# Optimization experiments

Hardware: AMD Instinct MI355X
Metric: run time of the kernel (lower is better)

The kernel has to match this reference:

```python
import jax, jax.numpy as jnp
import numpy as np

N_POINTS = 50000
IN_DIM = 16
HID = 64
HEADS = 4
SCALE = 1
NEG_SLOPE = 0.2  # PyG GATConv default
DELTAS = [1, 3, 5, 7, 9, 11]


def _make_graphs(n, scale):
    # edge_index_1: edges (i-d, i); edge_index_2: edges (i+d, i); edge_index_3: both
    e1 = np.concatenate([np.stack([np.arange(d * scale, n) - d * scale,
                                   np.arange(d * scale, n)]) for d in DELTAS], axis=1)
    e2 = np.concatenate([np.stack([np.arange(n - d * scale) + d * scale,
                                   np.arange(n - d * scale)]) for d in DELTAS], axis=1)
    e3 = np.concatenate([e1, e2], axis=1)
    return (jnp.asarray(e1, dtype=jnp.int64), jnp.asarray(e2, dtype=jnp.int64),
            jnp.asarray(e3, dtype=jnp.int64))


def setup_inputs() -> dict:
    key = jax.random.key(0)
    ks = jax.random.split(key, 16)
    e1, e2, e3 = _make_graphs(N_POINTS, SCALE)
    HC = HEADS * HID

    def g(k, shape, fan_in):
        return jax.random.normal(k, shape, dtype=jnp.float32) * (1.0 / np.sqrt(fan_in))

    return {
        "x": jax.random.normal(ks[0], (N_POINTS, IN_DIM), dtype=jnp.float32),
        "edge_index_1": e1,
        "edge_index_2": e2,
        "edge_index_3": e3,
        # stacked params for the 3 branches (leading dim 3)
        "W1": g(ks[1], (3, IN_DIM, HC), IN_DIM),
        "a1_src": g(ks[2], (3, HEADS, HID), HID),
        "a1_dst": g(ks[3], (3, HEADS, HID), HID),
        "b1": jnp.zeros((3, HC), dtype=jnp.float32),
        "W2": g(ks[4], (3, HC, HC), HC),
        "a2_src": g(ks[5], (3, HEADS, HID), HID),
        "a2_dst": g(ks[6], (3, HEADS, HID), HID),
        "b2": jnp.zeros((3, HID), dtype=jnp.float32),
        "W_fc": g(ks[7], (3, HID, 1), HID),
        "b_fc": jnp.zeros((3, 1), dtype=jnp.float32),
    }


def _gat(x, src, dst, W, a_src, a_dst, b, concat):
    """PyG GATConv: linear -> edge attention -> scatter-softmax -> scatter-add."""
    N = x.shape[0]
    H, C = a_src.shape
    h = (x @ W).reshape(N, H, C)                      # [N,H,C]
    # add self loops (PyG default add_self_loops=True; input graphs have none)
    loop = jnp.arange(N, dtype=src.dtype)
    src = jnp.concatenate([src, loop])
    dst = jnp.concatenate([dst, loop])
    alpha_s = (h * a_src).sum(-1)                     # [N,H]
    alpha_d = (h * a_dst).sum(-1)                     # [N,H]
    e = jax.nn.leaky_relu(alpha_s[src] + alpha_d[dst], NEG_SLOPE)  # [E,H]
    m = jax.ops.segment_max(e, dst, num_segments=N)   # per-dst max (stable softmax)
    ex = jnp.exp(e - m[dst])
    den = jax.ops.segment_sum(ex, dst, num_segments=N)
    alpha = ex / den[dst]                             # [E,H]
    out = jax.ops.segment_sum(alpha[:, :, None] * h[src], dst, num_segments=N)  # [N,H,C]
    out = out.reshape(N, H * C) if concat else out.mean(axis=1)
    return out + b


def reference(x, edge_index_1, edge_index_2, edge_index_3,
              W1, a1_src, a1_dst, b1, W2, a2_src, a2_dst, b2, W_fc, b_fc):
    eis = [edge_index_1, edge_index_2, edge_index_3]
    outs = []
    for k in range(3):
        src, dst = eis[k][0], eis[k][1]
        h = _gat(x, src, dst, W1[k], a1_src[k], a1_dst[k], b1[k], concat=True)
        h = _gat(h, src, dst, W2[k], a2_src[k], a2_dst[k], b2[k], concat=False)
        outs.append(h @ W_fc[k] + b_fc[k])            # [N,1]
    return tuple(outs)  # training-mode output (x1, x2, x3)
```

## Files before the change

kernel.cpp:

```cpp
#include <hip/hip_runtime.h>

#define NPTS 50000
#define NEG 0.2f
#define PSTRIDE 960
#define OUT_N 64
#define SPAN 86
#define SP 87
#define LOG2E 1.44269504088896340736f

typedef unsigned short u16;
typedef unsigned int   u32;

__device__ __forceinline__ float bf2f(u16 u){ return __uint_as_float(((u32)u) << 16); }
__device__ __forceinline__ u16 f2bf(float f){
  u32 w = __float_as_uint(f);
  return (u16)((w + 0x7fffu + ((w >> 16) & 1u)) >> 16);
}
__device__ __forceinline__ u32 pk2(float a, float b){
  return (u32)f2bf(a) | ((u32)f2bf(b) << 16);
}
__device__ __forceinline__ float ldraw(const void* p, long i, int isf32){
  return isf32 ? ((const float*)p)[i] : bf2f(((const u16*)p)[i]);
}
__device__ __forceinline__ float wred(float v){
  #pragma unroll
  for (int m = 32; m > 0; m >>= 1) v += __shfl_xor(v, m, 64);
  return v;
}

__device__ int detect_isf32(const void* x){
  int lane = threadIdx.x & 63;
  const u16* p = (const u16*)x;
  int ze = 0, sane = 0;
  #pragma unroll
  for (int r = 0; r < 8; r++){
    int idx = lane * 8 + r;
    u16 u = p[idx];
    if ((idx & 1) == 0 && u == 0) ze++;
    float a = fabsf(bf2f(u));
    if (u == 0 || (a > 0.015625f && a < 64.f)) sane++;
  }
  #pragma unroll
  for (int m = 32; m > 0; m >>= 1){ ze += __shfl_xor(ze, m, 64); sane += __shfl_xor(sane, m, 64); }
  return (ze > 200) ? 1 : (sane > 460 ? 0 : 1);
}

template<int B> __device__ __forceinline__ int nbr_off(int t){
  if (B == 0){ constexpr int O[7]  = {0,-1,-3,-5,-7,-9,-11}; return O[t]; }
  else if (B == 1){ constexpr int O[7]  = {0,1,3,5,7,9,11}; return O[t]; }
  else { constexpr int O[13] = {0,-1,1,-3,3,-5,5,-7,7,-9,9,-11,11}; return O[t]; }
}

__global__ __launch_bounds__(256) void k_fold1(const void* x, const void* W2, const void* a2s,
                                               const void* a2d, const void* wfc, float* sAg,
                                               int* flag){
  __shared__ int s_flag;
  if (threadIdx.x < 64){ int f = detect_isf32(x); if (threadIdx.x == 0) s_flag = f; }
  __syncthreads();
  int isf32 = s_flag;
  if (blockIdx.x == 0 && blockIdx.y == 0 && threadIdx.x == 0) *flag = isf32;
  int kb = blockIdx.y, m = blockIdx.x;
  int hp = threadIdx.x >> 6, ch = threadIdx.x & 63;
  int c = hp * 64 + ch;
  float w = ldraw(W2, (long)kb * 65536 + (long)m * 256 + c, isf32);
  float s = wred(w * ldraw(a2s, kb * 256 + c, isf32));
  float d = wred(w * ldraw(a2d, kb * 256 + c, isf32));
  float f = wred(w * ldraw(wfc, kb * 64 + ch, isf32) * 0.25f);
  if (ch == 0){
    float* sA = sAg + (long)kb * 3072;
    sA[(0 * 4 + hp) * 256 + m] = s;
    sA[(1 * 4 + hp) * 256 + m] = d;
    sA[(2 * 4 + hp) * 256 + m] = f;
  }
}

__global__ __launch_bounds__(256) void k_fold2(const void* x, const void* W1, const void* a1s,
                                               const void* a1d, const void* b1, const void* b2,
                                               const void* wfc, const void* bfc,
                                               const float* sAg, float* P){
  __shared__ int s_flag;
  if (threadIdx.x < 64){ int f = detect_isf32(x); if (threadIdx.x == 0) s_flag = f; }
  __syncthreads();
  int isf32 = s_flag;
  int kb = blockIdx.y;
  int wid = blockIdx.x * 4 + (threadIdx.x >> 6);
  int ch = threadIdx.x & 63;
  float* Pp = P + kb * PSTRIDE;
  const float* sA = sAg + (long)kb * 3072;

  if (wid < 256){
    int hp = wid & 3, h = (wid >> 2) & 3, k = wid >> 4;
    int m = h * 64 + ch;
    float w = ldraw(W1, (long)kb * 4096 + k * 256 + m, isf32);
    float s = wred(w * sA[(0 * 4 + hp) * 256 + m]);
    float d = wred(w * sA[(1 * 4 + hp) * 256 + m]);
    float f = wred(w * sA[(2 * 4 + hp) * 256 + m]);
    if (ch == 0){ Pp[128 + wid] = s; Pp[384 + wid] = d; Pp[640 + wid] = f; }
  } else if (wid < 320){
    int j = wid - 256; int h = j & 3, k = j >> 2;
    int c = h * 64 + ch;
    float w = ldraw(W1, (long)kb * 4096 + k * 256 + c, isf32);
    float s = wred(w * ldraw(a1s, kb * 256 + c, isf32));
    float d = wred(w * ldraw(a1d, kb * 256 + c, isf32));
    if (ch == 0){ Pp[j] = s; Pp[64 + j] = d; }
  } else if (wid < 324){
    int hp = wid - 320;
    float a0 = 0.f, a1v = 0.f, a2v = 0.f;
    for (int it = 0; it < 4; it++){
      int m = it * 64 + ch;
      float bv = ldraw(b1, kb * 256 + m, isf32);
      a0  += bv * sA[(0 * 4 + hp) * 256 + m];
      a1v += bv * sA[(1 * 4 + hp) * 256 + m];
      a2v += bv * sA[(2 * 4 + hp) * 256 + m];
    }
    a0 = wred(a0); a1v = wred(a1v); a2v = wred(a2v);
    if (ch == 0){ Pp[896 + hp] = a0; Pp[900 + hp] = a1v; Pp[904 + hp] = a2v; }
  } else if (wid == 324){
    float a = wred(ldraw(b2, kb * 64 + ch, isf32) * ldraw(wfc, kb * 64 + ch, isf32));
    if (ch == 0) Pp[908] = a + ldraw(bfc, kb, isf32);
  }
}

template<int BRANCH>
__device__ __forceinline__ void run_ab(const void* x, const float* Pp, int isf32, int base,
                                       float (&fe8)[8][SP], u32 (&feG)[4][SP * 7], float* o2b){
  constexpr int CNT = (BRANCH == 2) ? 13 : 7;
  int tid = threadIdx.x;

  if (tid < SPAN){
    int g = base - 11 + tid;
    bool vA = (unsigned)g < NPTS;
    float xv[16];
    if (vA){
      if (isf32){
        const float4* xp = (const float4*)x + (long)g * 4;
        #pragma unroll
        for (int q = 0; q < 4; q++){
          float4 v = xp[q];
          xv[q*4] = v.x; xv[q*4+1] = v.y; xv[q*4+2] = v.z; xv[q*4+3] = v.w;
        }
      } else {
        const uint4* xp = (const uint4*)x + (long)g * 2;
        #pragma unroll
        for (int q = 0; q < 2; q++){
          uint4 v = xp[q];
          u32 wsv[4] = {v.x, v.y, v.z, v.w};
          #pragma unroll
          for (int r = 0; r < 4; r++){
            xv[q*8 + r*2]     = bf2f((u16)(wsv[r] & 0xffffu));
            xv[q*8 + r*2 + 1] = bf2f((u16)(wsv[r] >> 16));
          }
        }
      }
    } else {
      #pragma unroll
      for (int k = 0; k < 16; k++) xv[k] = 0.f;
    }
    float s1[4] = {0,0,0,0}, d1[4] = {0,0,0,0};
    float s2[16], d2[16], f2[16];
    #pragma unroll
    for (int t = 0; t < 16; t++){ s2[t] = 0.f; d2[t] = 0.f; f2[t] = 0.f; }
    #pragma unroll
    for (int k = 0; k < 16; k++){
      float xk = xv[k];
      #pragma unroll
      for (int h = 0; h < 4; h++){
        s1[h] += xk * Pp[     k*4 + h];
        d1[h] += xk * Pp[64 + k*4 + h];
      }
      #pragma unroll
      for (int t = 0; t < 16; t++){
        s2[t] += xk * Pp[128 + k*16 + t];
        d2[t] += xk * Pp[384 + k*16 + t];
        f2[t] += xk * Pp[640 + k*16 + t];
      }
    }
    #pragma unroll
    for (int h = 0; h < 4; h++){
      fe8[h][tid]     = s1[h] * LOG2E;
      fe8[4 + h][tid] = d1[h] * LOG2E;
      u32* gp = &feG[h][tid * 7];
      gp[0] = pk2(s2[h*4+0], s2[h*4+1]);
      gp[1] = pk2(s2[h*4+2], s2[h*4+3]);
      gp[2] = pk2(d2[h*4+0], d2[h*4+1]);
      gp[3] = pk2(d2[h*4+2], d2[h*4+3]);
      gp[4] = pk2(f2[h*4+0], f2[h*4+1]);
      gp[5] = pk2(f2[h*4+2], f2[h*4+3]);
    }
  }
  __syncthreads();

  #pragma unroll
  for (int pass = 0; pass < 2; pass++){
    int task = pass * 128 + tid;
    int noff = task >> 2, h = task & 3;
    int i = base + noff;
    bool vB = i < NPTS;
    float ts[4] = {0,0,0,0}, td[4] = {0,0,0,0}, tf[4] = {0,0,0,0};
    if (vB){
      int sAs = noff + 11;
      float adv = fe8[4 + h][sAs];
      float e[CNT]; int sa[CNT];
      float mx = -3e38f;
      #pragma unroll
      for (int tt = 0; tt < CNT; tt++){
        int off = nbr_off<BRANCH>(tt);
        int j = i + off;
        sa[tt] = sAs + off;
        float v = fe8[h][sa[tt]] + adv;
        v = v > 0.f ? v : NEG * v;
        e[tt] = ((unsigned)j < NPTS) ? v : -3e38f;
        mx = fmaxf(mx, e[tt]);
      }
      float den = 0.f;
      #pragma unroll
      for (int tt = 0; tt < CNT; tt++){
        float ex = exp2f(e[tt] - mx);
        den += ex;
        const u32* gp = &feG[h][sa[tt] * 7];
        u32 g0 = gp[0], g1 = gp[1], g2 = gp[2], g3 = gp[3], g4 = gp[4], g5 = gp[5];
        ts[0] += ex * bf2f((u16)(g0 & 0xffffu)); ts[1] += ex * bf2f((u16)(g0 >> 16));
        ts[2] += ex * bf2f((u16)(g1 & 0xffffu)); ts[3] += ex * bf2f((u16)(g1 >> 16));
        td[0] += ex * bf2f((u16)(g2 & 0xffffu)); td[1] += ex * bf2f((u16)(g2 >> 16));
        td[2] += ex * bf2f((u16)(g3 & 0xffffu)); td[3] += ex * bf2f((u16)(g3 >> 16));
        tf[0] += ex * bf2f((u16)(g4 & 0xffffu)); tf[1] += ex * bf2f((u16)(g4 >> 16));
        tf[2] += ex * bf2f((u16)(g5 & 0xffffu)); tf[3] += ex * bf2f((u16)(g5 >> 16));
      }
      float inv = 1.f / den;
      #pragma unroll
      for (int hp = 0; hp < 4; hp++){ ts[hp] *= inv; td[hp] *= inv; tf[hp] *= inv; }
    }
    #pragma unroll
    for (int hp = 0; hp < 4; hp++){
      ts[hp] += __shfl_xor(ts[hp], 1, 64); ts[hp] += __shfl_xor(ts[hp], 2, 64);
      td[hp] += __shfl_xor(td[hp], 1, 64); td[hp] += __shfl_xor(td[hp], 2, 64);
      tf[hp] += __shfl_xor(tf[hp], 1, 64); tf[hp] += __shfl_xor(tf[hp], 2, 64);
    }
    if (h == 0 && vB){
      float* ob = o2b + (long)i * 12;
      *(float4*)(ob + 0) = make_float4((ts[0] + Pp[896]) * LOG2E, (ts[1] + Pp[897]) * LOG2E,
                                       (ts[2] + Pp[898]) * LOG2E, (ts[3] + Pp[899]) * LOG2E);
      *(float4*)(ob + 4) = make_float4((td[0] + Pp[900]) * LOG2E, (td[1] + Pp[901]) * LOG2E,
                                       (td[2] + Pp[902]) * LOG2E, (td[3] + Pp[903]) * LOG2E);
      *(float4*)(ob + 8) = make_float4(tf[0] + Pp[904], tf[1] + Pp[905],
                                       tf[2] + Pp[906], tf[3] + Pp[907]);
    }
  }
}

__global__ __launch_bounds__(128) void k_AB(const void* x, const float* P, const int* flag,
                                            float* o2g){
  __shared__ float fe8[8][SP];
  __shared__ u32 feG[4][SP * 7];
  int br = blockIdx.y;
  int isf32 = *flag;
  const float* Pp = P + br * PSTRIDE;
  float* o2b = o2g + (long)br * NPTS * 12;
  int base = blockIdx.x * OUT_N;
  if (br == 0)      run_ab<0>(x, Pp, isf32, base, fe8, feG, o2b);
  else if (br == 1) run_ab<1>(x, Pp, isf32, base, fe8, feG, o2b);
  else              run_ab<2>(x, Pp, isf32, base, fe8, feG, o2b);
}

template<int BRANCH>
__device__ __forceinline__ void run_c(const float* ob, const float* Pp, int isf32, long t,
                                      void* out){
  constexpr int CNT = (BRANCH == 2) ? 13 : 7;
  int node = (int)(t >> 2), hp = (int)(t & 3);
  if (node >= NPTS) return;
  float adv = ob[(long)node * 12 + 4 + hp];
  float e[CNT]; int jc[CNT];
  float mx = -3e38f;
  #pragma unroll
  for (int tt = 0; tt < CNT; tt++){
    int off = nbr_off<BRANCH>(tt);
    int j = node + off;
    int jj = j < 0 ? 0 : (j >= NPTS ? NPTS - 1 : j);
    jc[tt] = jj;
    float v = ob[(long)jj * 12 + hp] + adv;
    v = v > 0.f ? v : NEG * v;
    e[tt] = ((unsigned)j < NPTS) ? v : -3e38f;
    mx = fmaxf(mx, e[tt]);
  }
  float den = 0.f, sm = 0.f;
  #pragma unroll
  for (int tt = 0; tt < CNT; tt++){
    float ex = exp2f(e[tt] - mx);
    den += ex;
    sm += ex * ob[(long)jc[tt] * 12 + 8 + hp];
  }
  float r = sm / den;
  r += __shfl_xor(r, 1, 64);
  r += __shfl_xor(r, 2, 64);
  if (hp == 0){
    float o = r + Pp[908];
    long oi = (long)BRANCH * NPTS + node;
    if (isf32) ((float*)out)[oi] = o;
    else       ((u16*)out)[oi]  = f2bf(o);
  }
}

__global__ __launch_bounds__(256) void k_C(const float* o2g, const float* P, const int* flag,
                                           void* out){
  long t = (long)blockIdx.x * 256 + threadIdx.x;
  int br = blockIdx.y;
  int isf32 = *flag;
  const float* ob = o2g + (long)br * NPTS * 12;
  const float* Pp = P + br * PSTRIDE;
  if (br == 0)      run_c<0>(ob, Pp, isf32, t, out);
  else if (br == 1) run_c<1>(ob, Pp, isf32, t, out);
  else              run_c<2>(ob, Pp, isf32, t, out);
}

extern "C" void kernel_launch(void* const* d_in, const int* in_sizes, int n_in,
                              void* d_out, int out_size, void* d_ws, size_t ws_size,
                              hipStream_t stream){
  char* ws = (char*)d_ws;
  size_t off = 0;
  auto take = [&](size_t b) -> size_t { size_t r = off; off += (b + 255) & ~(size_t)255; return r; };

  float* sAg  = (float*)(ws + take((size_t)3 * 3072 * 4));
  float* P    = (float*)(ws + take((size_t)3 * PSTRIDE * 4));
  int*   flag = (int*)(ws + take(4));
  float* o2g  = (float*)(ws + take((size_t)3 * NPTS * 12 * 4));

  const void* x   = d_in[0];
  const void* W1  = d_in[4];
  const void* a1s = d_in[5];
  const void* a1d = d_in[6];
  const void* b1  = d_in[7];
  const void* W2  = d_in[8];
  const void* a2s = d_in[9];
  const void* a2d = d_in[10];
  const void* b2  = d_in[11];
  const void* wfc = d_in[12];
  const void* bfc = d_in[13];

  k_fold1<<<dim3(256, 3), 256, 0, stream>>>(x, W2, a2s, a2d, wfc, sAg, flag);
  k_fold2<<<dim3(82, 3), 256, 0, stream>>>(x, W1, a1s, a1d, b1, b2, wfc, bfc, sAg, P);
  k_AB<<<dim3((NPTS + OUT_N - 1) / OUT_N, 3), 128, 0, stream>>>(x, P, flag, o2g);
  k_C<<<dim3((NPTS * 4 + 255) / 256, 3), 256, 0, stream>>>(o2g, P, flag, d_out);
}
```

Before: 58.94 us.

## Split fused halo-tile AB kernel into per-node feature kernel and gather kernel

Replaces the shared-memory tiled k_AB kernel, which recomputed node features over an 86-node halo for every 64 outputs and used only 128 threads, with two kernels. k_feat computes each node's projected features once and writes them to a global workspace as fp32 attention logits plus packed bf16 values. k_B then gathers neighbor features from global memory, one thread per node-head. The aim is to remove the halo recomputation and raise occupancy, at the cost of an extra launch and a global round trip of about 19 MB. The bf16 packing and unpacking also switch to hardware intrinsics and mask-based shifts.

New measurement: 56.62 us. 1.04x faster.

```diff
diff --git a/kernel.cpp b/kernel.cpp
--- a/kernel.cpp
+++ b/kernel.cpp
@@ -1,11 +1,9 @@
 #include <hip/hip_runtime.h>
+#include <hip/hip_bf16.h>
 
 #define NPTS 50000
 #define NEG 0.2f
 #define PSTRIDE 960
-#define OUT_N 64
-#define SPAN 86
-#define SP 87
 #define LOG2E 1.44269504088896340736f
 
 typedef unsigned short u16;
@@ -17,8 +15,12 @@
   return (u16)((w + 0x7fffu + ((w >> 16) & 1u)) >> 16);
 }
 __device__ __forceinline__ u32 pk2(float a, float b){
-  return (u32)f2bf(a) | ((u32)f2bf(b) << 16);
-}
+  __hip_bfloat162 h2 = __float22bfloat162_rn(float2{a, b});
+  union { __hip_bfloat162 h; u32 u; } cv; cv.h = h2;
+  return cv.u;
+}
+__device__ __forceinline__ float ulo(u32 g){ return __uint_as_float(g << 16); }
+__device__ __forceinline__ float uhi(u32 g){ return __uint_as_float(g & 0xffff0000u); }
 __device__ __forceinline__ float ldraw(const void* p, long i, int isf32){
   return isf32 ? ((const float*)p)[i] : bf2f(((const u16*)p)[i]);
 }
@@ -121,145 +123,145 @@
   }
 }
 
-template<int BRANCH>
-__device__ __forceinline__ void run_ab(const void* x, const float* Pp, int isf32, int base,
-                                       float (&fe8)[8][SP], u32 (&feG)[4][SP * 7], float* o2b){
-  constexpr int CNT = (BRANCH == 2) ? 13 : 7;
-  int tid = threadIdx.x;
-
-  if (tid < SPAN){
-    int g = base - 11 + tid;
-    bool vA = (unsigned)g < NPTS;
-    float xv[16];
-    if (vA){
-      if (isf32){
-        const float4* xp = (const float4*)x + (long)g * 4;
-        #pragma unroll
-        for (int q = 0; q < 4; q++){
-          float4 v = xp[q];
-          xv[q*4] = v.x; xv[q*4+1] = v.y; xv[q*4+2] = v.z; xv[q*4+3] = v.w;
-        }
-      } else {
-        const uint4* xp = (const uint4*)x + (long)g * 2;
-        #pragma unroll
-        for (int q = 0; q < 2; q++){
-          uint4 v = xp[q];
-          u32 wsv[4] = {v.x, v.y, v.z, v.w};
-          #pragma unroll
-          for (int r = 0; r < 4; r++){
-            xv[q*8 + r*2]     = bf2f((u16)(wsv[r] & 0xffffu));
-            xv[q*8 + r*2 + 1] = bf2f((u16)(wsv[r] >> 16));
-          }
-        }
+__global__ __launch_bounds__(256) void k_feat(const void* x, const float* P, const int* flag,
+                                              u32* Fg){
+  int node = blockIdx.x * 256 + threadIdx.x;
+  if (node >= NPTS) return;
+  int kb = blockIdx.y;
+  int isf32 = *flag;
+  const float* Pp = P + kb * PSTRIDE;
+
+  float xv[16];
+  if (isf32){
+    const float4* xp = (const float4*)x + (long)node * 4;
+    #pragma unroll
+    for (int q = 0; q < 4; q++){
+      float4 v = xp[q];
+      xv[q*4] = v.x; xv[q*4+1] = v.y; xv[q*4+2] = v.z; xv[q*4+3] = v.w;
+    }
+  } else {
+    const uint4* xp = (const uint4*)x + (long)node * 2;
+    #pragma unroll
+    for (int q = 0; q < 2; q++){
+      uint4 v = xp[q];
+      u32 wsv[4] = {v.x, v.y, v.z, v.w};
+      #pragma unroll
+      for (int r = 0; r < 4; r++){
+        xv[q*8 + r*2]     = ulo(wsv[r]);
+        xv[q*8 + r*2 + 1] = uhi(wsv[r]);
       }
-    } else {
-      #pragma unroll
-      for (int k = 0; k < 16; k++) xv[k] = 0.f;
-    }
-    float s1[4] = {0,0,0,0}, d1[4] = {0,0,0,0};
-    float s2[16], d2[16], f2[16];
-    #pragma unroll
-    for (int t = 0; t < 16; t++){ s2[t] = 0.f; d2[t] = 0.f; f2[t] = 0.f; }
-    #pragma unroll
-    for (int k = 0; k < 16; k++){
-      float xk = xv[k];
-      #pragma unroll
-      for (int h = 0; h < 4; h++){
-        s1[h] += xk * Pp[     k*4 + h];
-        d1[h] += xk * Pp[64 + k*4 + h];
-      }
-      #pragma unroll
-      for (int t = 0; t < 16; t++){
-        s2[t] += xk * Pp[128 + k*16 + t];
-        d2[t] += xk * Pp[384 + k*16 + t];
-        f2[t] += xk * Pp[640 + k*16 + t];
-      }
-    }
+    }
+  }
+
+  float s1[4] = {0,0,0,0}, d1[4] = {0,0,0,0};
+  float s2[16], d2[16], f2[16];
+  #pragma unroll
+  for (int t = 0; t < 16; t++){ s2[t] = 0.f; d2[t] = 0.f; f2[t] = 0.f; }
+  #pragma unroll
+  for (int k = 0; k < 16; k++){
+    float xk = xv[k];
     #pragma unroll
     for (int h = 0; h < 4; h++){
-      fe8[h][tid]     = s1[h] * LOG2E;
-      fe8[4 + h][tid] = d1[h] * LOG2E;
-      u32* gp = &feG[h][tid * 7];
-      gp[0] = pk2(s2[h*4+0], s2[h*4+1]);
-      gp[1] = pk2(s2[h*4+2], s2[h*4+3]);
-      gp[2] = pk2(d2[h*4+0], d2[h*4+1]);
-      gp[3] = pk2(d2[h*4+2], d2[h*4+3]);
-      gp[4] = pk2(f2[h*4+0], f2[h*4+1]);
-      gp[5] = pk2(f2[h*4+2], f2[h*4+3]);
-    }
-  }
-  __syncthreads();
-
-  #pragma unroll
-  for (int pass = 0; pass < 2; pass++){
-    int task = pass * 128 + tid;
-    int noff = task >> 2, h = task & 3;
-    int i = base + noff;
-    bool vB = i < NPTS;
-    float ts[4] = {0,0,0,0}, td[4] = {0,0,0,0}, tf[4] = {0,0,0,0};
-    if (vB){
-      int sAs = noff + 11;
-      float adv = fe8[4 + h][sAs];
-      float e[CNT]; int sa[CNT];
-      float mx = -3e38f;
-      #pragma unroll
-      for (int tt = 0; tt < CNT; tt++){
-        int off = nbr_off<BRANCH>(tt);
-        int j = i + off;
-        sa[tt] = sAs + off;
-        float v = fe8[h][sa[tt]] + adv;
-        v = v > 0.f ? v : NEG * v;
-        e[tt] = ((unsigned)j < NPTS) ? v : -3e38f;
-        mx = fmaxf(mx, e[tt]);
-      }
-      float den = 0.f;
-      #pragma unroll
-      for (int tt = 0; tt < CNT; tt++){
-        float ex = exp2f(e[tt] - mx);
-        den += ex;
-        const u32* gp = &feG[h][sa[tt] * 7];
-        u32 g0 = gp[0], g1 = gp[1], g2 = gp[2], g3 = gp[3], g4 = gp[4], g5 = gp[5];
-        ts[0] += ex * bf2f((u16)(g0 & 0xffffu)); ts[1] += ex * bf2f((u16)(g0 >> 16));
-        ts[2] += ex * bf2f((u16)(g1 & 0xffffu)); ts[3] += ex * bf2f((u16)(g1 >> 16));
-        td[0] += ex * bf2f((u16)(g2 & 0xffffu)); td[1] += ex * bf2f((u16)(g2 >> 16));
-        td[2] += ex * bf2f((u16)(g3 & 0xffffu)); td[3] += ex * bf2f((u16)(g3 >> 16));
-        tf[0] += ex * bf2f((u16)(g4 & 0xffffu)); tf[1] += ex * bf2f((u16)(g4 >> 16));
-        tf[2] += ex * bf2f((u16)(g5 & 0xffffu)); tf[3] += ex * bf2f((u16)(g5 >> 16));
-      }
-      float inv = 1.f / den;
-      #pragma unroll
-      for (int hp = 0; hp < 4; hp++){ ts[hp] *= inv; td[hp] *= inv; tf[hp] *= inv; }
+      s1[h] += xk * Pp[     k*4 + h];
+      d1[h] += xk * Pp[64 + k*4 + h];
     }
     #pragma unroll
-    for (int hp = 0; hp < 4; hp++){
-      ts[hp] += __shfl_xor(ts[hp], 1, 64); ts[hp] += __shfl_xor(ts[hp], 2, 64);
-      td[hp] += __shfl_xor(td[hp], 1, 64); td[hp] += __shfl_xor(td[hp], 2, 64);
-      tf[hp] += __shfl_xor(tf[hp], 1, 64); tf[hp] += __shfl_xor(tf[hp], 2, 64);
-    }
-    if (h == 0 && vB){
-      float* ob = o2b + (long)i * 12;
-      *(float4*)(ob + 0) = make_float4((ts[0] + Pp[896]) * LOG2E, (ts[1] + Pp[897]) * LOG2E,
-                                       (ts[2] + Pp[898]) * LOG2E, (ts[3] + Pp[899]) * LOG2E);
-      *(float4*)(ob + 4) = make_float4((td[0] + Pp[900]) * LOG2E, (td[1] + Pp[901]) * LOG2E,
-                                       (td[2] + Pp[902]) * LOG2E, (td[3] + Pp[903]) * LOG2E);
-      *(float4*)(ob + 8) = make_float4(tf[0] + Pp[904], tf[1] + Pp[905],
-                                       tf[2] + Pp[906], tf[3] + Pp[907]);
-    }
-  }
-}
-
-__global__ __launch_bounds__(128) void k_AB(const void* x, const float* P, const int* flag,
-                                            float* o2g){
-  __shared__ float fe8[8][SP];
-  __shared__ u32 feG[4][SP * 7];
+    for (int t = 0; t < 16; t++){
+      s2[t] += xk * Pp[128 + k*16 + t];
+      d2[t] += xk * Pp[384 + k*16 + t];
+      f2[t] += xk * Pp[640 + k*16 + t];
+    }
+  }
+
+  u32* F = Fg + (long)kb * NPTS * 16 + (long)node * 16;
+  uint4 w0 = {__float_as_uint(s1[0] * LOG2E), __float_as_uint(s1[1] * LOG2E),
+              __float_as_uint(s1[2] * LOG2E), __float_as_uint(s1[3] * LOG2E)};
+  uint4 w1 = {__float_as_uint(d1[0] * LOG2E), __float_as_uint(d1[1] * LOG2E),
+              __float_as_uint(d1[2] * LOG2E), __float_as_uint(d1[3] * LOG2E)};
+  *(uint4*)(F + 0) = w0;
+  *(uint4*)(F + 4) = w1;
+  uint4 w2 = {pk2(s2[0], s2[1]), pk2(s2[2], s2[3]), pk2(s2[4], s2[5]), pk2(s2[6], s2[7])};
+  uint4 w3 = {pk2(s2[8], s2[9]), pk2(s2[10], s2[11]), pk2(s2[12], s2[13]), pk2(s2[14], s2[15])};
+  *(uint4*)(F + 8)  = w2;
+  *(uint4*)(F + 12) = w3;
+  u32* G = Fg + (long)3 * NPTS * 16 + (long)kb * NPTS * 16 + (long)node * 16;
+  uint4 w4 = {pk2(d2[0], d2[1]), pk2(d2[2], d2[3]), pk2(d2[4], d2[5]), pk2(d2[6], d2[7])};
+  uint4 w5 = {pk2(d2[8], d2[9]), pk2(d2[10], d2[11]), pk2(d2[12], d2[13]), pk2(d2[14], d2[15])};
+  uint4 w6 = {pk2(f2[0], f2[1]), pk2(f2[2], f2[3]), pk2(f2[4], f2[5]), pk2(f2[6], f2[7])};
+  uint4 w7 = {pk2(f2[8], f2[9]), pk2(f2[10], f2[11]), pk2(f2[12], f2[13]), pk2(f2[14], f2[15])};
+  *(uint4*)(G + 0)  = w4;
+  *(uint4*)(G + 4)  = w5;
+  *(uint4*)(G + 8)  = w6;
+  *(uint4*)(G + 12) = w7;
+}
+
+template<int BRANCH>
+__device__ __forceinline__ void run_b(const u32* F, const u32* G, const float* Pp, long t,
+                                      float* o2b){
+  constexpr int CNT = (BRANCH == 2) ? 13 : 7;
+  int node = (int)(t >> 2), h = (int)(t & 3);
+  if (node >= NPTS) return;
+  float adv = __uint_as_float(F[(long)node * 16 + 4 + h]);
+
+  float e[CNT]; int jc[CNT];
+  float mx = -3e38f;
+  #pragma unroll
+  for (int tt = 0; tt < CNT; tt++){
+    int off = nbr_off<BRANCH>(tt);
+    int j = node + off;
+    int jj = j < 0 ? 0 : (j >= NPTS ? NPTS - 1 : j);
+    jc[tt] = jj;
+    float v = __uint_as_float(F[(long)jj * 16 + h]) + adv;
+    v = v > 0.f ? v : NEG * v;
+    e[tt] = ((unsigned)j < NPTS) ? v : -3e38f;
+    mx = fmaxf(mx, e[tt]);
+  }
+  float den = 0.f;
+  float ts[4] = {0,0,0,0}, td[4] = {0,0,0,0}, tf[4] = {0,0,0,0};
+  #pragma unroll
+  for (int tt = 0; tt < CNT; tt++){
+    float ex = exp2f(e[tt] - mx);
+    den += ex;
+    long fb = (long)jc[tt] * 16;
+    u32 gs0 = F[fb + 8 + h * 2], gs1 = F[fb + 9 + h * 2];
+    u32 gd0 = G[fb + h * 2],     gd1 = G[fb + 1 + h * 2];
+    u32 gf0 = G[fb + 8 + h * 2], gf1 = G[fb + 9 + h * 2];
+    ts[0] += ex * ulo(gs0); ts[1] += ex * uhi(gs0);
+    ts[2] += ex * ulo(gs1); ts[3] += ex * uhi(gs1);
+    td[0] += ex * ulo(gd0); td[1] += ex * uhi(gd0);
+    td[2] += ex * ulo(gd1); td[3] += ex * uhi(gd1);
+    tf[0] += ex * ulo(gf0); tf[1] += ex * uhi(gf0);
+    tf[2] += ex * ulo(gf1); tf[3] += ex * uhi(gf1);
+  }
+  float inv = 1.f / den;
+  #pragma unroll
+  for (int hp = 0; hp < 4; hp++){
+    ts[hp] *= inv; td[hp] *= inv; tf[hp] *= inv;
+    ts[hp] += __shfl_xor(ts[hp], 1, 64); ts[hp] += __shfl_xor(ts[hp], 2, 64);
+    td[hp] += __shfl_xor(td[hp], 1, 64); td[hp] += __shfl_xor(td[hp], 2, 64);
+    tf[hp] += __shfl_xor(tf[hp], 1, 64); tf[hp] += __shfl_xor(tf[hp], 2, 64);
+  }
+  if (h == 0){
+    float* ob = o2b + (long)node * 12;
+    *(float4*)(ob + 0) = make_float4((ts[0] + Pp[896]) * LOG2E, (ts[1] + Pp[897]) * LOG2E,
+                                     (ts[2] + Pp[898]) * LOG2E, (ts[3] + Pp[899]) * LOG2E);
+    *(float4*)(ob + 4) = make_float4((td[0] + Pp[900]) * LOG2E, (td[1] + Pp[901]) * LOG2E,
+                                     (td[2] + Pp[902]) * LOG2E, (td[3] + Pp[903]) * LOG2E);
+    *(float4*)(ob + 8) = make_float4(tf[0] + Pp[904], tf[1] + Pp[905],
+                                     tf[2] + Pp[906], tf[3] + Pp[907]);
+  }
+}
+
+__global__ __launch_bounds__(256) void k_B(const u32* Fg, const float* P, float* o2g){
+  long t = (long)blockIdx.x * 256 + threadIdx.x;
   int br = blockIdx.y;
-  int isf32 = *flag;
+  const u32* F = Fg + (long)br * NPTS * 16;
+  const u32* G = Fg + (long)3 * NPTS * 16 + (long)br * NPTS * 16;
   const float* Pp = P + br * PSTRIDE;
   float* o2b = o2g + (long)br * NPTS * 12;
-  int base = blockIdx.x * OUT_N;
-  if (br == 0)      run_ab<0>(x, Pp, isf32, base, fe8, feG, o2b);
-  else if (br == 1) run_ab<1>(x, Pp, isf32, base, fe8, feG, o2b);
-  else              run_ab<2>(x, Pp, isf32, base, fe8, feG, o2b);
+  if (br == 0)      run_b<0>(F, G, Pp, t, o2b);
+  else if (br == 1) run_b<1>(F, G, Pp, t, o2b);
+  else              run_b<2>(F, G, Pp, t, o2b);
 }
 
 template<int BRANCH>
@@ -322,6 +324,7 @@
   float* sAg  = (float*)(ws + take((size_t)3 * 3072 * 4));
   float* P    = (float*)(ws + take((size_t)3 * PSTRIDE * 4));
   int*   flag = (int*)(ws + take(4));
+  u32*   Fg   = (u32*)(ws + take((size_t)6 * NPTS * 16 * 4));
   float* o2g  = (float*)(ws + take((size_t)3 * NPTS * 12 * 4));
 
   const void* x   = d_in[0];
@@ -338,6 +341,7 @@
 
   k_fold1<<<dim3(256, 3), 256, 0, stream>>>(x, W2, a2s, a2d, wfc, sAg, flag);
   k_fold2<<<dim3(82, 3), 256, 0, stream>>>(x, W1, a1s, a1d, b1, b2, wfc, bfc, sAg, P);
-  k_AB<<<dim3((NPTS + OUT_N - 1) / OUT_N, 3), 128, 0, stream>>>(x, P, flag, o2g);
+  k_feat<<<dim3((NPTS + 255) / 256, 3), 256, 0, stream>>>(x, P, flag, Fg);
+  k_B<<<dim3((NPTS * 4 + 255) / 256, 3), 256, 0, stream>>>(Fg, P, o2g);
   k_C<<<dim3((NPTS * 4 + 255) / 256, 3), 256, 0, stream>>>(o2g, P, flag, d_out);
 }
```
